# Kernel tuning notes

Hardware: AMD Instinct MI355X
Metric: run time of the kernel (lower is better)

The kernel has to match this reference:

```python
import jax, jax.numpy as jnp
from jax import lax
import numpy as np

B, C, HH, WW = 8, 64, 128, 128
N = HH * WW
EPS = 1e-5


def _roll_h(xn, sign):
    # per-channel cyclic roll along H: out[b,c,h,w] = xn[b,c,(h - sign*c) % H, w]
    _, Cx, Hx, _ = xn.shape
    c = jnp.arange(Cx)[:, None]
    idx = (jnp.arange(Hx)[None, :] - sign * jnp.arange(Cx)[:, None]) % Hx  # (C,H)
    return xn[:, c, idx, :]


def _roll_w(xn, sign):
    return _roll_h(xn.transpose(0, 1, 3, 2), sign).transpose(0, 1, 3, 2)


def _ch_linear(xn, w, b):
    # nn.Linear over the channel dim of a BCHW tensor (token-MLP on (B,N,C))
    return jnp.einsum('bchw,cd->bdhw', xn, w) + b[None, :, None, None]


def _bn(xn, g, b):
    # BatchNorm2d, training-mode stats (biased var over B,H,W)
    m = xn.mean(axis=(0, 2, 3), keepdims=True)
    v = xn.var(axis=(0, 2, 3), keepdims=True)
    return (xn - m) * lax.rsqrt(v + EPS) * g[None, :, None, None] + b[None, :, None, None]


def _dwconv(xn, w, dil, pad):
    return lax.conv_general_dilated(xn, w, (1, 1), ((pad, pad), (pad, pad)),
                                    rhs_dilation=(dil, dil),
                                    dimension_numbers=('NCHW', 'OIHW', 'NCHW'),
                                    feature_group_count=xn.shape[1])


def _pc(xn, w):
    # 1x1 pointwise conv, no bias; w: (C_out, C_in)
    return jnp.einsum('bchw,oc->bohw', xn, w)


def lgff_forward(x, fc1_w, fc1_b, fc2_w, fc2_b, fc3_w, fc3_b, fc4_w, fc4_b,
                 fc5_w, fc5_b, ln_g, ln_b, pc_w, dw_w, dw_b, dw_bn_g, dw_bn_b,
                 dd_w, dd_bn_g, dd_bn_b, se_w1, se_b1, se_w2, se_b2, H, W):
    Bx, Nx, Cx = x.shape
    xn = x.transpose(0, 2, 1).reshape(Bx, Cx, H, W)
    # branch 1: roll+c along H -> fc1 -> GELU -> roll+c along W -> fc2
    a = jax.nn.gelu(_ch_linear(_roll_h(xn, 1), fc1_w, fc1_b), approximate=False)
    x_1 = _ch_linear(_roll_w(a, 1), fc2_w, fc2_b) + xn
    # branch 2: roll-c along W -> fc3 -> GELU -> roll+c along H -> fc4
    b = jax.nn.gelu(_ch_linear(_roll_w(xn, -1), fc3_w, fc3_b), approximate=False)
    x_2 = _ch_linear(_roll_h(b, 1), fc4_w, fc4_b) + xn
    # concat along feature dim (token layout dim=2 == channel dim here), LayerNorm(2C), fc5
    xc = jnp.concatenate([x_1, x_2], axis=1)  # (B, 2C, H, W)
    m = xc.mean(axis=1, keepdims=True)
    v = xc.var(axis=1, keepdims=True)
    xc = (xc - m) * lax.rsqrt(v + EPS) * ln_g[None, :, None, None] + ln_b[None, :, None, None]
    x1 = _ch_linear(xc, fc5_w, fc5_b) + xn
    # conv fusion part
    x2 = _pc(x1, pc_w)
    y = jax.nn.relu(_bn(_dwconv(x2, dw_w, 1, 1) + dw_b[None, :, None, None], dw_bn_g, dw_bn_b))
    y = jax.nn.relu(_bn(_dwconv(y, dd_w, 2, 2), dd_bn_g, dd_bn_b))
    y = _pc(y, pc_w)
    # four branches x3..x6 share identical weights/input -> identical outputs
    x7 = 4.0 * (x2 * y)
    # SE block
    s = x7.mean(axis=(2, 3), keepdims=True)  # (B,C,1,1)
    e = jax.nn.relu(jnp.einsum('bcij,oc->boij', s, se_w1) + se_b1[None, :, None, None])
    e = jax.nn.sigmoid(jnp.einsum('bcij,oc->boij', e, se_w2) + se_b2[None, :, None, None])
    return x7 + x7 * e  # (B, C, H, W)


def setup_inputs():
    key = jax.random.key(0)
    ks = jax.random.split(key, 12)
    r = C // 8
    inp = {
        'x': jax.random.normal(ks[0], (B, N, C), jnp.float32),
        'fc1_w': jax.random.normal(ks[1], (C, C), jnp.float32) * 0.02,
        'fc1_b': jnp.zeros((C,), jnp.float32),
        'fc2_w': jax.random.normal(ks[2], (C, C), jnp.float32) * 0.02,
        'fc2_b': jnp.zeros((C,), jnp.float32),
        'fc3_w': jax.random.normal(ks[3], (C, C), jnp.float32) * 0.02,
        'fc3_b': jnp.zeros((C,), jnp.float32),
        'fc4_w': jax.random.normal(ks[4], (C, C), jnp.float32) * 0.02,
        'fc4_b': jnp.zeros((C,), jnp.float32),
        'fc5_w': jax.random.normal(ks[5], (2 * C, C), jnp.float32) * 0.02,
        'fc5_b': jnp.zeros((C,), jnp.float32),
        'ln_g': jnp.ones((2 * C,), jnp.float32),
        'ln_b': jnp.zeros((2 * C,), jnp.float32),
        'pc_w': jax.random.normal(ks[6], (C, C), jnp.float32) * np.sqrt(2.0 / C).astype(np.float32),
        'dw_w': jax.random.normal(ks[7], (C, 1, 3, 3), jnp.float32) * np.sqrt(2.0 / 9.0).astype(np.float32),
        'dw_b': jnp.zeros((C,), jnp.float32),
        'dw_bn_g': jnp.ones((C,), jnp.float32),
        'dw_bn_b': jnp.zeros((C,), jnp.float32),
        'dd_w': jax.random.normal(ks[8], (C, 1, 3, 3), jnp.float32) * np.sqrt(2.0 / 9.0).astype(np.float32),
        'dd_bn_g': jnp.ones((C,), jnp.float32),
        'dd_bn_b': jnp.zeros((C,), jnp.float32),
        'se_w1': jax.random.normal(ks[9], (r, C), jnp.float32) * np.sqrt(2.0 / r).astype(np.float32),
        'se_b1': jnp.zeros((r,), jnp.float32),
        'se_w2': jax.random.normal(ks[10], (C, r), jnp.float32) * np.sqrt(2.0 / C).astype(np.float32),
        'se_b2': jnp.zeros((C,), jnp.float32),
        'H': HH,
        'W': WW,
    }
    return inp


def reference(x, fc1_w, fc1_b, fc2_w, fc2_b, fc3_w, fc3_b, fc4_w, fc4_b,
              fc5_w, fc5_b, ln_g, ln_b, pc_w, dw_w, dw_b, dw_bn_g, dw_bn_b,
              dd_w, dd_bn_g, dd_bn_b, se_w1, se_b1, se_w2, se_b2, H, W):
    return lgff_forward(x, fc1_w, fc1_b, fc2_w, fc2_b, fc3_w, fc3_b, fc4_w, fc4_b,
                        fc5_w, fc5_b, ln_g, ln_b, pc_w, dw_w, dw_b, dw_bn_g, dw_bn_b,
                        dd_w, dd_bn_g, dd_bn_b, se_w1, se_b1, se_w2, se_b2, H, W)
```

## Files before the change

kernel.cpp:

```cpp
#include <hip/hip_runtime.h>

constexpr int NB  = 8;
constexpr int NC  = 64;
constexpr int NH  = 128;
constexpr int NW  = 128;
constexpr int NHW = NH * NW;
constexpr int CHW = NC * NHW;
constexpr int SZ  = NB * CHW;
constexpr int NPOS = NB * NHW;
constexpr float EPS = 1e-5f;

typedef unsigned short u16;
using bf8   = __attribute__((ext_vector_type(8))) short;
using u16x8 = __attribute__((ext_vector_type(8))) u16;
using f32x4 = __attribute__((ext_vector_type(4))) float;

static __device__ inline short f2bf(float f) {
    union { float f; unsigned int u; } v; v.f = f;
    unsigned int r = v.u + 0x7fffu + ((v.u >> 16) & 1u);
    return (short)(r >> 16);
}
static __device__ inline float bf2f(u16 u) {
    union { unsigned int i; float f; } v; v.i = ((unsigned int)u) << 16;
    return v.f;
}

__global__ void k_transpose(const float* __restrict__ x, u16* __restrict__ xn) {
    __shared__ float t[64 * 65];
    int b   = blockIdx.x >> 8;
    int hw0 = (blockIdx.x & 255) << 6;
    int tid = threadIdx.x;
    #pragma unroll
    for (int k = 0; k < 16; ++k) {
        int idx = tid + (k << 8);
        int c = idx & 63, hwl = idx >> 6;
        t[c * 65 + hwl] = x[((size_t)b * NHW + hw0 + hwl) * NC + c];
    }
    __syncthreads();
    #pragma unroll
    for (int k = 0; k < 16; ++k) {
        int idx = tid + (k << 8);
        int hwl = idx & 63, c = idx >> 6;
        xn[(size_t)(b * NC + c) * NHW + hw0 + hwl] = (u16)f2bf(t[c * 65 + hwl]);
    }
}

template<int MODE, bool GELU_OUT, bool WTRANS, bool HASBIAS, bool BNRELU_IN>
__global__ __launch_bounds__(256) void
k_mfc(const u16* __restrict__ in, const float* __restrict__ wgt,
      const float* __restrict__ bias,
      const float* __restrict__ meanc, const float* __restrict__ rstdc,
      const float* __restrict__ bng, const float* __restrict__ bnb,
      u16* __restrict__ out) {
    __shared__ short wt[64 * 64];
    __shared__ float scl[64], sft[64];
    int tid = threadIdx.x;
    int l = tid & 63, wv = tid >> 6;

    if (!WTRANS) {
        #pragma unroll
        for (int i = 0; i < 8; ++i) {
            int c0 = wv * 2 + i * 8;
            unsigned int pk = (unsigned int)(u16)f2bf(wgt[c0 * 64 + l]) |
                              ((unsigned int)(u16)f2bf(wgt[(c0 + 1) * 64 + l]) << 16);
            *(unsigned int*)&wt[l * 64 + (c0 ^ ((l & 7) << 3))] = pk;
        }
    } else {
        #pragma unroll
        for (int i = 0; i < 16; ++i) {
            int d = wv * 16 + i;
            wt[d * 64 + (l ^ ((d & 7) << 3))] = f2bf(wgt[d * 64 + l]);
        }
    }
    if (BNRELU_IN && tid < 64) {
        float s = rstdc[tid] * bng[tid];
        scl[tid] = s;
        sft[tid] = bnb[tid] - meanc[tid] * s;
    }
    __syncthreads();

    int q = l >> 4, col = l & 15;
    int p  = blockIdx.x * 64 + wv * 16 + col;
    int b  = p >> 14;
    int hw = p & (NHW - 1);
    int h  = hw >> 7, w = hw & 127;
    const u16* inb = in + (size_t)b * CHW;

    f32x4 acc[4];
    #pragma unroll
    for (int dt = 0; dt < 4; ++dt) acc[dt] = (f32x4){0.f, 0.f, 0.f, 0.f};

    #pragma unroll
    for (int ks = 0; ks < 2; ++ks) {
        bf8 bfr;
        #pragma unroll
        for (int j = 0; j < 8; ++j) {
            int c = ks * 32 + q * 8 + j;
            int addr;
            if (MODE == 0)      addr = c * NHW + (((h - c) & 127) << 7) + w;
            else if (MODE == 1) addr = c * NHW + (h << 7) + ((w - c) & 127);
            else if (MODE == 2) addr = c * NHW + (h << 7) + ((w + c) & 127);
            else                addr = c * NHW + hw;
            u16 raw = inb[addr];
            if (BNRELU_IN) {
                float v = fmaxf(bf2f(raw) * scl[c] + sft[c], 0.f);
                bfr[j] = f2bf(v);
            } else {
                bfr[j] = (short)raw;
            }
        }
        #pragma unroll
        for (int dt = 0; dt < 4; ++dt) {
            int d = dt * 16 + col;
            bf8 afr = *(bf8*)&wt[d * 64 + ((ks * 32 + q * 8) ^ ((d & 7) << 3))];
            acc[dt] = __builtin_amdgcn_mfma_f32_16x16x32_bf16(afr, bfr, acc[dt], 0, 0, 0);
        }
    }

    size_t obase = (size_t)b * CHW + hw;
    #pragma unroll
    for (int dt = 0; dt < 4; ++dt) {
        #pragma unroll
        for (int r = 0; r < 4; ++r) {
            int d = dt * 16 + q * 4 + r;
            float val = acc[dt][r];
            if (HASBIAS) val += bias[d];
            if (GELU_OUT) val = 0.5f * val * (1.f + erff(val * 0.70710678118654752f));
            out[obase + (size_t)d * NHW] = (u16)f2bf(val);
        }
    }
}

__global__ void k_pq(const float* __restrict__ w5, const float* __restrict__ lng,
                     const float* __restrict__ lnb, float* __restrict__ PQ) {
    int d = threadIdx.x;
    float P = 0.f, Q = 0.f;
    for (int c = 0; c < 128; ++c) {
        float wv = w5[c * 64 + d];
        P += lng[c] * wv;
        Q += lnb[c] * wv;
    }
    PQ[d] = P; PQ[64 + d] = Q;
}

__global__ __launch_bounds__(256) void
k_ffuse(const u16* __restrict__ t1, const u16* __restrict__ t2,
        const u16* __restrict__ xnb,
        const float* __restrict__ fc2w, const float* __restrict__ fc2b,
        const float* __restrict__ fc4w, const float* __restrict__ fc4b,
        const float* __restrict__ w5, const float* __restrict__ lng,
        const float* __restrict__ PQ, const float* __restrict__ b5,
        u16* __restrict__ x1out) {
    __shared__ short wA[64 * 64];
    __shared__ short wB[64 * 64];
    __shared__ short wG[64 * 128];
    __shared__ short xt[64 * 136];

    int tid = threadIdx.x;
    int l = tid & 63, wv = tid >> 6;

    #pragma unroll
    for (int i = 0; i < 8; ++i) {
        int c0 = wv * 2 + i * 8;
        unsigned int pa = (unsigned int)(u16)f2bf(fc2w[c0 * 64 + l]) |
                          ((unsigned int)(u16)f2bf(fc2w[(c0 + 1) * 64 + l]) << 16);
        *(unsigned int*)&wA[l * 64 + (c0 ^ ((l & 7) << 3))] = pa;
        unsigned int pb = (unsigned int)(u16)f2bf(fc4w[c0 * 64 + l]) |
                          ((unsigned int)(u16)f2bf(fc4w[(c0 + 1) * 64 + l]) << 16);
        *(unsigned int*)&wB[l * 64 + (c0 ^ ((l & 7) << 3))] = pb;
    }
    #pragma unroll
    for (int i = 0; i < 16; ++i) {
        int c0 = wv * 2 + i * 8;
        unsigned int pk = (unsigned int)(u16)f2bf(lng[c0] * w5[c0 * 64 + l]) |
                          ((unsigned int)(u16)f2bf(lng[c0 + 1] * w5[(c0 + 1) * 64 + l]) << 16);
        *(unsigned int*)&wG[l * 128 + (c0 ^ ((l & 7) << 3))] = pk;
    }
    __syncthreads();

    int q = l >> 4, col = l & 15;
    int p  = blockIdx.x * 64 + wv * 16 + col;
    int b  = p >> 14;
    int hw = p & (NHW - 1);
    int h  = hw >> 7, w = hw & 127;
    size_t base = (size_t)b * CHW;
    int pos = wv * 16 + col;

    f32x4 acc1[4], acc2[4];
    #pragma unroll
    for (int dt = 0; dt < 4; ++dt) {
        acc1[dt] = (f32x4){0.f, 0.f, 0.f, 0.f};
        acc2[dt] = (f32x4){0.f, 0.f, 0.f, 0.f};
    }
    #pragma unroll
    for (int ks = 0; ks < 2; ++ks) {
        bf8 f1, f2;
        #pragma unroll
        for (int j = 0; j < 8; ++j) {
            int c = ks * 32 + q * 8 + j;
            f1[j] = (short)t1[base + c * NHW + (h << 7) + ((w - c) & 127)];
            f2[j] = (short)t2[base + c * NHW + (((h - c) & 127) << 7) + w];
        }
        #pragma unroll
        for (int dt = 0; dt < 4; ++dt) {
            int d = dt * 16 + col;
            int wo = (ks * 32 + q * 8) ^ ((d & 7) << 3);
            acc1[dt] = __builtin_amdgcn_mfma_f32_16x16x32_bf16(*(bf8*)&wA[d * 64 + wo], f1, acc1[dt], 0, 0, 0);
            acc2[dt] = __builtin_amdgcn_mfma_f32_16x16x32_bf16(*(bf8*)&wB[d * 64 + wo], f2, acc2[dt], 0, 0, 0);
        }
    }

    float xr[16];
    #pragma unroll
    for (int dt = 0; dt < 4; ++dt)
        #pragma unroll
        for (int r = 0; r < 4; ++r)
            xr[dt * 4 + r] = bf2f(xnb[base + (size_t)(dt * 16 + q * 4 + r) * NHW + hw]);

    float s = 0.f, sq = 0.f;
    #pragma unroll
    for (int dt = 0; dt < 4; ++dt) {
        float v1[4], v2[4];
        #pragma unroll
        for (int r = 0; r < 4; ++r) {
            int d = dt * 16 + q * 4 + r;
            v1[r] = acc1[dt][r] + fc2b[d] + xr[dt * 4 + r];
            v2[r] = acc2[dt][r] + fc4b[d] + xr[dt * 4 + r];
            s += v1[r] + v2[r];
            sq += v1[r] * v1[r] + v2[r] * v2[r];
        }
        unsigned int pk0 = (unsigned int)(u16)f2bf(v1[0]) | ((unsigned int)(u16)f2bf(v1[1]) << 16);
        unsigned int pk1 = (unsigned int)(u16)f2bf(v1[2]) | ((unsigned int)(u16)f2bf(v1[3]) << 16);
        *(uint2*)&xt[pos * 136 + dt * 16 + q * 4] = make_uint2(pk0, pk1);
        unsigned int pk2 = (unsigned int)(u16)f2bf(v2[0]) | ((unsigned int)(u16)f2bf(v2[1]) << 16);
        unsigned int pk3 = (unsigned int)(u16)f2bf(v2[2]) | ((unsigned int)(u16)f2bf(v2[3]) << 16);
        *(uint2*)&xt[pos * 136 + 64 + dt * 16 + q * 4] = make_uint2(pk2, pk3);
    }
    s  += __shfl_xor(s, 16);  s += __shfl_xor(s, 32);
    sq += __shfl_xor(sq, 16); sq += __shfl_xor(sq, 32);
    float m    = s * (1.f / 128.f);
    float var  = sq * (1.f / 128.f) - m * m;
    float rstd = rsqrtf(var + EPS);
    float mr   = m * rstd;
    __syncthreads();

    f32x4 acc[4];
    #pragma unroll
    for (int dt = 0; dt < 4; ++dt) acc[dt] = (f32x4){0.f, 0.f, 0.f, 0.f};
    #pragma unroll
    for (int ks = 0; ks < 4; ++ks) {
        bf8 bfr = *(bf8*)&xt[pos * 136 + ks * 32 + q * 8];
        #pragma unroll
        for (int dt = 0; dt < 4; ++dt) {
            int d = dt * 16 + col;
            bf8 afr = *(bf8*)&wG[d * 128 + ((ks * 32 + q * 8) ^ ((d & 7) << 3))];
            acc[dt] = __builtin_amdgcn_mfma_f32_16x16x32_bf16(afr, bfr, acc[dt], 0, 0, 0);
        }
    }

    size_t obase = base + hw;
    #pragma unroll
    for (int dt = 0; dt < 4; ++dt) {
        #pragma unroll
        for (int r = 0; r < 4; ++r) {
            int d = dt * 16 + q * 4 + r;
            float val = rstd * acc[dt][r] + PQ[64 + d] - mr * PQ[d] + b5[d] + xr[dt * 4 + r];
            x1out[obase + (size_t)d * NHW] = (u16)f2bf(val);
        }
    }
}

template<int DIL, bool HASBIAS, bool BNIN>
__global__ __launch_bounds__(256) void
k_dwlds(const u16* __restrict__ in, const float* __restrict__ wgt,
        const float* __restrict__ bias,
        const float* __restrict__ meanc, const float* __restrict__ rstdc,
        const float* __restrict__ bng, const float* __restrict__ bnb,
        u16* __restrict__ out, float* __restrict__ psum, float* __restrict__ psq) {
    constexpr int STR = 136;
    __shared__ float tile[36 * STR];
    __shared__ float ss[256], sq[256];

    int blk = ((blockIdx.x & 7) << 8) | (blockIdx.x >> 3);
    int q   = blk & 3;
    int bc  = blk >> 2;
    int c   = bc & 63;
    int r0  = q * 32;
    int tid = threadIdx.x;
    const u16* ip = in + (size_t)bc * NHW;

    float scale = 0.f, shift = 0.f;
    if (BNIN) { scale = rstdc[c] * bng[c]; shift = bnb[c] - meanc[c] * scale; }

    #pragma unroll 1
    for (int idx = tid; idx < 36 * 16; idx += 256) {
        int lr = idx >> 4, u = idx & 15;
        int gr = r0 - 2 + lr;
        float v[8] = {0.f, 0.f, 0.f, 0.f, 0.f, 0.f, 0.f, 0.f};
        if (gr >= 0 && gr < NH) {
            u16x8 raw = *(const u16x8*)(ip + gr * NW + u * 8);
            #pragma unroll
            for (int j = 0; j < 8; ++j) {
                float f = bf2f(raw[j]);
                if (BNIN) f = fmaxf(f * scale + shift, 0.f);
                v[j] = f;
            }
        }
        *(float4*)&tile[lr * STR + 4 + u * 8]     = make_float4(v[0], v[1], v[2], v[3]);
        *(float4*)&tile[lr * STR + 4 + u * 8 + 4] = make_float4(v[4], v[5], v[6], v[7]);
        if (u == 0)  *(float4*)&tile[lr * STR]       = make_float4(0.f, 0.f, 0.f, 0.f);
        if (u == 15) *(float4*)&tile[lr * STR + 132] = make_float4(0.f, 0.f, 0.f, 0.f);
    }
    __syncthreads();

    float wc[9];
    #pragma unroll
    for (int k = 0; k < 9; ++k) wc[k] = wgt[c * 9 + k];

    int row  = tid >> 3;
    int col0 = (tid & 7) * 16;
    float o[16];
    float bb = HASBIAS ? bias[c] : 0.f;
    #pragma unroll
    for (int j = 0; j < 16; ++j) o[j] = bb;

    #pragma unroll
    for (int i = 0; i < 3; ++i) {
        const float* rp = &tile[(row + 2 + (i - 1) * DIL) * STR + 4 + col0];
        float4 A  = *(const float4*)(rp - 4);
        float4 B0 = *(const float4*)(rp);
        float4 B1 = *(const float4*)(rp + 4);
        float4 B2 = *(const float4*)(rp + 8);
        float4 B3 = *(const float4*)(rp + 12);
        float4 Cc = *(const float4*)(rp + 16);
        float ww[24] = {A.x,A.y,A.z,A.w, B0.x,B0.y,B0.z,B0.w, B1.x,B1.y,B1.z,B1.w,
                        B2.x,B2.y,B2.z,B2.w, B3.x,B3.y,B3.z,B3.w, Cc.x,Cc.y,Cc.z,Cc.w};
        float w0 = wc[3 * i], w1 = wc[3 * i + 1], w2 = wc[3 * i + 2];
        #pragma unroll
        for (int j = 0; j < 16; ++j)
            o[j] += w0 * ww[4 + j - DIL] + w1 * ww[4 + j] + w2 * ww[4 + j + DIL];
    }

    u16* op = out + (size_t)bc * NHW + (r0 + row) * NW + col0;
    u16x8 o1, o2;
    #pragma unroll
    for (int j = 0; j < 8; ++j) { o1[j] = (u16)f2bf(o[j]); o2[j] = (u16)f2bf(o[8 + j]); }
    *(u16x8*)(op)     = o1;
    *(u16x8*)(op + 8) = o2;

    float s = 0.f, qq = 0.f;
    #pragma unroll
    for (int j = 0; j < 16; ++j) { s += o[j]; qq += o[j] * o[j]; }
    ss[tid] = s; sq[tid] = qq; __syncthreads();
    for (int off = 128; off > 0; off >>= 1) {
        if (tid < off) { ss[tid] += ss[tid + off]; sq[tid] += sq[tid + off]; }
        __syncthreads();
    }
    if (tid == 0) { psum[blk] = ss[0]; psq[blk] = sq[0]; }
}

__global__ void k_bn_finalize(const float* __restrict__ psum, const float* __restrict__ psq,
                              float* __restrict__ meanc, float* __restrict__ rstdc) {
    int c = threadIdx.x;
    float s = 0.f, qv = 0.f;
    for (int b = 0; b < NB; ++b)
        #pragma unroll
        for (int j = 0; j < 4; ++j) {
            int idx = ((b * 64 + c) << 2) + j;
            s += psum[idx]; qv += psq[idx];
        }
    const float inv = 1.f / (float)(NB * NHW);
    float m = s * inv;
    float v = qv * inv - m * m;
    meanc[c] = m;
    rstdc[c] = rsqrtf(v + EPS);
}

__global__ void k_se_reduce(const u16* __restrict__ x2, const u16* __restrict__ y3,
                            float* __restrict__ s4) {
    __shared__ float ss[256];
    int q   = blockIdx.x & 3;
    int bc  = blockIdx.x >> 2;
    int tid = threadIdx.x;
    const u16* a  = x2 + (size_t)bc * NHW + q * (NHW / 4);
    const u16* b_ = y3 + (size_t)bc * NHW + q * (NHW / 4);
    float acc = 0.f;
    #pragma unroll
    for (int i = 0; i < 2; ++i) {
        u16x8 av = *(const u16x8*)(a + (tid + i * 256) * 8);
        u16x8 bv = *(const u16x8*)(b_ + (tid + i * 256) * 8);
        #pragma unroll
        for (int j = 0; j < 8; ++j) acc += bf2f(av[j]) * bf2f(bv[j]);
    }
    ss[tid] = acc; __syncthreads();
    for (int o = 128; o > 0; o >>= 1) {
        if (tid < o) ss[tid] += ss[tid + o];
        __syncthreads();
    }
    if (tid == 0) s4[blockIdx.x] = ss[0];
}

__global__ void k_se_mlp(const float* __restrict__ s4, const float* __restrict__ w1,
                         const float* __restrict__ b1, const float* __restrict__ w2,
                         const float* __restrict__ b2, float* __restrict__ e) {
    __shared__ float sh[64], e1[8];
    int b = blockIdx.x, tid = threadIdx.x;
    float sv = 0.f;
    #pragma unroll
    for (int j = 0; j < 4; ++j) sv += s4[(b * 64 + tid) * 4 + j];
    sh[tid] = sv * (4.f / (float)NHW);
    __syncthreads();
    if (tid < 8) {
        float a = b1[tid];
        for (int c = 0; c < 64; ++c) a += sh[c] * w1[tid * 64 + c];
        e1[tid] = a > 0.f ? a : 0.f;
    }
    __syncthreads();
    float a = b2[tid];
    #pragma unroll
    for (int j = 0; j < 8; ++j) a += e1[j] * w2[tid * 8 + j];
    e[b * 64 + tid] = 1.f / (1.f + expf(-a));
}

__global__ void k_final8(const u16* __restrict__ x2, const u16* __restrict__ y3,
                         const float* __restrict__ e, float* __restrict__ out) {
    int t  = blockIdx.x * 256 + threadIdx.x;
    int bc = t >> 11;
    float f = 4.f * (1.f + e[bc]);
    u16x8 av = *(const u16x8*)(x2 + (size_t)t * 8);
    u16x8 bv = *(const u16x8*)(y3 + (size_t)t * 8);
    float4 o0, o1;
    o0.x = f * bf2f(av[0]) * bf2f(bv[0]); o0.y = f * bf2f(av[1]) * bf2f(bv[1]);
    o0.z = f * bf2f(av[2]) * bf2f(bv[2]); o0.w = f * bf2f(av[3]) * bf2f(bv[3]);
    o1.x = f * bf2f(av[4]) * bf2f(bv[4]); o1.y = f * bf2f(av[5]) * bf2f(bv[5]);
    o1.z = f * bf2f(av[6]) * bf2f(bv[6]); o1.w = f * bf2f(av[7]) * bf2f(bv[7]);
    *(float4*)(out + (size_t)t * 8)     = o0;
    *(float4*)(out + (size_t)t * 8 + 4) = o1;
}

extern "C" void kernel_launch(void* const* d_in, const int* in_sizes, int n_in,
                              void* d_out, int out_size, void* d_ws, size_t ws_size,
                              hipStream_t stream) {
    const float* x     = (const float*)d_in[0];
    const float* fc1w  = (const float*)d_in[1];
    const float* fc1b  = (const float*)d_in[2];
    const float* fc2w  = (const float*)d_in[3];
    const float* fc2b  = (const float*)d_in[4];
    const float* fc3w  = (const float*)d_in[5];
    const float* fc3b  = (const float*)d_in[6];
    const float* fc4w  = (const float*)d_in[7];
    const float* fc4b  = (const float*)d_in[8];
    const float* fc5w  = (const float*)d_in[9];
    const float* fc5b  = (const float*)d_in[10];
    const float* lng   = (const float*)d_in[11];
    const float* lnb   = (const float*)d_in[12];
    const float* pcw   = (const float*)d_in[13];
    const float* dww   = (const float*)d_in[14];
    const float* dwb   = (const float*)d_in[15];
    const float* dwbng = (const float*)d_in[16];
    const float* dwbnb = (const float*)d_in[17];
    const float* ddw   = (const float*)d_in[18];
    const float* ddbng = (const float*)d_in[19];
    const float* ddbnb = (const float*)d_in[20];
    const float* sew1  = (const float*)d_in[21];
    const float* seb1  = (const float*)d_in[22];
    const float* sew2  = (const float*)d_in[23];
    const float* seb2  = (const float*)d_in[24];

    float* out = (float*)d_out;
    u16* wsu = (u16*)d_ws;
    u16* bufA = wsu;
    u16* bufB = wsu + (size_t)SZ;
    u16* bufC = wsu + (size_t)2 * SZ;
    u16* bufD = wsu + (size_t)3 * SZ;
    float* st = (float*)(wsu + (size_t)4 * SZ);
    float* psumA  = st;
    float* psqA   = st + 2048;
    float* meanc1 = st + 4096;
    float* rstdc1 = st + 4160;
    float* meanc2 = st + 4224;
    float* rstdc2 = st + 4288;
    float* svec   = st + 4352;
    float* evec   = st + 6400;
    float* pqv    = st + 6912;

    dim3 blk(256);
    const float* nil = nullptr;

    k_transpose<<<NB * (NHW / 64), blk, 0, stream>>>(x, bufA);
    k_pq<<<1, 64, 0, stream>>>(fc5w, lng, lnb, pqv);
    k_mfc<0, true,  false, true, false><<<NPOS / 64, blk, 0, stream>>>(bufA, fc1w, fc1b, nil, nil, nil, nil, bufB);
    k_mfc<2, true,  false, true, false><<<NPOS / 64, blk, 0, stream>>>(bufA, fc3w, fc3b, nil, nil, nil, nil, bufC);
    k_ffuse<<<NPOS / 64, blk, 0, stream>>>(bufB, bufC, bufA, fc2w, fc2b, fc4w, fc4b,
                                           fc5w, lng, pqv, fc5b, bufD);
    k_mfc<3, false, true, false, false><<<NPOS / 64, blk, 0, stream>>>(bufD, pcw, nil, nil, nil, nil, nil, bufA);
    k_dwlds<1, true, false><<<2048, blk, 0, stream>>>(bufA, dww, dwb, nil, nil, nil, nil, bufB, psumA, psqA);
    k_bn_finalize<<<1, 64, 0, stream>>>(psumA, psqA, meanc1, rstdc1);
    k_dwlds<2, false, true><<<2048, blk, 0, stream>>>(bufB, ddw, nil, meanc1, rstdc1, dwbng, dwbnb, bufC, psumA, psqA);
    k_bn_finalize<<<1, 64, 0, stream>>>(psumA, psqA, meanc2, rstdc2);
    k_mfc<3, false, true, false, true><<<NPOS / 64, blk, 0, stream>>>(bufC, pcw, nil, meanc2, rstdc2, ddbng, ddbnb, bufD);
    k_se_reduce<<<NB * NC * 4, blk, 0, stream>>>(bufA, bufD, svec);
    k_se_mlp<<<NB, 64, 0, stream>>>(svec, sew1, seb1, sew2, seb2, evec);
    k_final8<<<SZ / 2048, blk, 0, stream>>>(bufA, bufD, evec, out);
}
```

Before: 152.8 us.

## Fuse fc1/fc3 into one kernel and fold pointwise conv into ffuse

Merges the two roll+fc+GELU kernels into a single kernel that reads the input once and writes both intermediates. It also appends the 1x1 pointwise conv to the fused fc2/fc4/LayerNorm/fc5 kernel, reusing shared memory for the pc weights so the fc5 output never goes to global memory. Kernel launches and intermediate global traffic both drop. The trade-off is higher register and LDS pressure per block, plus an extra sync, which may lower occupancy.

New measurement: 191.1 us. +25.0%, slower.

```diff
diff --git a/kernel.cpp b/kernel.cpp
--- a/kernel.cpp
+++ b/kernel.cpp
@@ -45,92 +45,6 @@
     }
 }
 
-template<int MODE, bool GELU_OUT, bool WTRANS, bool HASBIAS, bool BNRELU_IN>
-__global__ __launch_bounds__(256) void
-k_mfc(const u16* __restrict__ in, const float* __restrict__ wgt,
-      const float* __restrict__ bias,
-      const float* __restrict__ meanc, const float* __restrict__ rstdc,
-      const float* __restrict__ bng, const float* __restrict__ bnb,
-      u16* __restrict__ out) {
-    __shared__ short wt[64 * 64];
-    __shared__ float scl[64], sft[64];
-    int tid = threadIdx.x;
-    int l = tid & 63, wv = tid >> 6;
-
-    if (!WTRANS) {
-        #pragma unroll
-        for (int i = 0; i < 8; ++i) {
-            int c0 = wv * 2 + i * 8;
-            unsigned int pk = (unsigned int)(u16)f2bf(wgt[c0 * 64 + l]) |
-                              ((unsigned int)(u16)f2bf(wgt[(c0 + 1) * 64 + l]) << 16);
-            *(unsigned int*)&wt[l * 64 + (c0 ^ ((l & 7) << 3))] = pk;
-        }
-    } else {
-        #pragma unroll
-        for (int i = 0; i < 16; ++i) {
-            int d = wv * 16 + i;
-            wt[d * 64 + (l ^ ((d & 7) << 3))] = f2bf(wgt[d * 64 + l]);
-        }
-    }
-    if (BNRELU_IN && tid < 64) {
-        float s = rstdc[tid] * bng[tid];
-        scl[tid] = s;
-        sft[tid] = bnb[tid] - meanc[tid] * s;
-    }
-    __syncthreads();
-
-    int q = l >> 4, col = l & 15;
-    int p  = blockIdx.x * 64 + wv * 16 + col;
-    int b  = p >> 14;
-    int hw = p & (NHW - 1);
-    int h  = hw >> 7, w = hw & 127;
-    const u16* inb = in + (size_t)b * CHW;
-
-    f32x4 acc[4];
-    #pragma unroll
-    for (int dt = 0; dt < 4; ++dt) acc[dt] = (f32x4){0.f, 0.f, 0.f, 0.f};
-
-    #pragma unroll
-    for (int ks = 0; ks < 2; ++ks) {
-        bf8 bfr;
-        #pragma unroll
-        for (int j = 0; j < 8; ++j) {
-            int c = ks * 32 + q * 8 + j;
-            int addr;
-            if (MODE == 0)      addr = c * NHW + (((h - c) & 127) << 7) + w;
-            else if (MODE == 1) addr = c * NHW + (h << 7) + ((w - c) & 127);
-            else if (MODE == 2) addr = c * NHW + (h << 7) + ((w + c) & 127);
-            else                addr = c * NHW + hw;
-            u16 raw = inb[addr];
-            if (BNRELU_IN) {
-                float v = fmaxf(bf2f(raw) * scl[c] + sft[c], 0.f);
-                bfr[j] = f2bf(v);
-            } else {
-                bfr[j] = (short)raw;
-            }
-        }
-        #pragma unroll
-        for (int dt = 0; dt < 4; ++dt) {
-            int d = dt * 16 + col;
-            bf8 afr = *(bf8*)&wt[d * 64 + ((ks * 32 + q * 8) ^ ((d & 7) << 3))];
-            acc[dt] = __builtin_amdgcn_mfma_f32_16x16x32_bf16(afr, bfr, acc[dt], 0, 0, 0);
-        }
-    }
-
-    size_t obase = (size_t)b * CHW + hw;
-    #pragma unroll
-    for (int dt = 0; dt < 4; ++dt) {
-        #pragma unroll
-        for (int r = 0; r < 4; ++r) {
-            int d = dt * 16 + q * 4 + r;
-            float val = acc[dt][r];
-            if (HASBIAS) val += bias[d];
-            if (GELU_OUT) val = 0.5f * val * (1.f + erff(val * 0.70710678118654752f));
-            out[obase + (size_t)d * NHW] = (u16)f2bf(val);
-        }
-    }
-}
-
 __global__ void k_pq(const float* __restrict__ w5, const float* __restrict__ lng,
                      const float* __restrict__ lnb, float* __restrict__ PQ) {
     int d = threadIdx.x;
@@ -144,17 +58,88 @@
 }
 
 __global__ __launch_bounds__(256) void
-k_ffuse(const u16* __restrict__ t1, const u16* __restrict__ t2,
-        const u16* __restrict__ xnb,
-        const float* __restrict__ fc2w, const float* __restrict__ fc2b,
-        const float* __restrict__ fc4w, const float* __restrict__ fc4b,
-        const float* __restrict__ w5, const float* __restrict__ lng,
-        const float* __restrict__ PQ, const float* __restrict__ b5,
-        u16* __restrict__ x1out) {
+k_mfc2(const u16* __restrict__ xn,
+       const float* __restrict__ w1, const float* __restrict__ b1,
+       const float* __restrict__ w3, const float* __restrict__ b3,
+       u16* __restrict__ t1, u16* __restrict__ t2) {
     __shared__ short wA[64 * 64];
     __shared__ short wB[64 * 64];
-    __shared__ short wG[64 * 128];
-    __shared__ short xt[64 * 136];
+    int tid = threadIdx.x;
+    int l = tid & 63, wv = tid >> 6;
+
+    #pragma unroll
+    for (int i = 0; i < 8; ++i) {
+        int c0 = wv * 2 + i * 8;
+        unsigned int pa = (unsigned int)(u16)f2bf(w1[c0 * 64 + l]) |
+                          ((unsigned int)(u16)f2bf(w1[(c0 + 1) * 64 + l]) << 16);
+        *(unsigned int*)&wA[l * 64 + (c0 ^ ((l & 7) << 3))] = pa;
+        unsigned int pb = (unsigned int)(u16)f2bf(w3[c0 * 64 + l]) |
+                          ((unsigned int)(u16)f2bf(w3[(c0 + 1) * 64 + l]) << 16);
+        *(unsigned int*)&wB[l * 64 + (c0 ^ ((l & 7) << 3))] = pb;
+    }
+    __syncthreads();
+
+    int q = l >> 4, col = l & 15;
+    int p  = blockIdx.x * 64 + wv * 16 + col;
+    int b  = p >> 14;
+    int hw = p & (NHW - 1);
+    int h  = hw >> 7, w = hw & 127;
+    const u16* inb = xn + (size_t)b * CHW;
+
+    f32x4 acc1[4], acc2[4];
+    #pragma unroll
+    for (int dt = 0; dt < 4; ++dt) {
+        acc1[dt] = (f32x4){0.f, 0.f, 0.f, 0.f};
+        acc2[dt] = (f32x4){0.f, 0.f, 0.f, 0.f};
+    }
+    #pragma unroll
+    for (int ks = 0; ks < 2; ++ks) {
+        bf8 f1, f2;
+        #pragma unroll
+        for (int j = 0; j < 8; ++j) {
+            int c = ks * 32 + q * 8 + j;
+            f1[j] = (short)inb[c * NHW + (((h - c) & 127) << 7) + w];
+            f2[j] = (short)inb[c * NHW + (h << 7) + ((w + c) & 127)];
+        }
+        #pragma unroll
+        for (int dt = 0; dt < 4; ++dt) {
+            int d = dt * 16 + col;
+            int wo = (ks * 32 + q * 8) ^ ((d & 7) << 3);
+            acc1[dt] = __builtin_amdgcn_mfma_f32_16x16x32_bf16(*(bf8*)&wA[d * 64 + wo], f1, acc1[dt], 0, 0, 0);
+            acc2[dt] = __builtin_amdgcn_mfma_f32_16x16x32_bf16(*(bf8*)&wB[d * 64 + wo], f2, acc2[dt], 0, 0, 0);
+        }
+    }
+
+    size_t obase = (size_t)b * CHW + hw;
+    #pragma unroll
+    for (int dt = 0; dt < 4; ++dt) {
+        #pragma unroll
+        for (int r = 0; r < 4; ++r) {
+            int d = dt * 16 + q * 4 + r;
+            float v1 = acc1[dt][r] + b1[d];
+            v1 = 0.5f * v1 * (1.f + erff(v1 * 0.70710678118654752f));
+            float v2 = acc2[dt][r] + b3[d];
+            v2 = 0.5f * v2 * (1.f + erff(v2 * 0.70710678118654752f));
+            t1[obase + (size_t)d * NHW] = (u16)f2bf(v1);
+            t2[obase + (size_t)d * NHW] = (u16)f2bf(v2);
+        }
+    }
+}
+
+__global__ __launch_bounds__(256) void
+k_ffusepc(const u16* __restrict__ t1, const u16* __restrict__ t2,
+          const u16* __restrict__ xnb,
+          const float* __restrict__ fc2w, const float* __restrict__ fc2b,
+          const float* __restrict__ fc4w, const float* __restrict__ fc4b,
+          const float* __restrict__ w5, const float* __restrict__ lng,
+          const float* __restrict__ PQ, const float* __restrict__ b5,
+          const float* __restrict__ pcw,
+          u16* __restrict__ x2out) {
+    __shared__ short smem[25088];
+    short* wA = smem;
+    short* wB = smem + 4096;
+    short* wG = smem + 8192;
+    short* xt = smem + 16384;
 
     int tid = threadIdx.x;
     int l = tid & 63, wv = tid >> 6;
@@ -242,7 +227,14 @@
     float var  = sq * (1.f / 128.f) - m * m;
     float rstd = rsqrtf(var + EPS);
     float mr   = m * rstd;
-    __syncthreads();
+
+    __syncthreads();
+    short* wP = wA;
+    #pragma unroll
+    for (int i = 0; i < 16; ++i) {
+        int d = wv * 16 + i;
+        wP[d * 64 + (l ^ ((d & 7) << 3))] = f2bf(pcw[d * 64 + l]);
+    }
 
     f32x4 acc[4];
     #pragma unroll
@@ -257,17 +249,108 @@
             acc[dt] = __builtin_amdgcn_mfma_f32_16x16x32_bf16(afr, bfr, acc[dt], 0, 0, 0);
         }
     }
-
-    size_t obase = base + hw;
+    __syncthreads();
+
     #pragma unroll
     for (int dt = 0; dt < 4; ++dt) {
+        float v[4];
         #pragma unroll
         for (int r = 0; r < 4; ++r) {
             int d = dt * 16 + q * 4 + r;
-            float val = rstd * acc[dt][r] + PQ[64 + d] - mr * PQ[d] + b5[d] + xr[dt * 4 + r];
-            x1out[obase + (size_t)d * NHW] = (u16)f2bf(val);
-        }
-    }
+            v[r] = rstd * acc[dt][r] + PQ[64 + d] - mr * PQ[d] + b5[d] + xr[dt * 4 + r];
+        }
+        unsigned int pk0 = (unsigned int)(u16)f2bf(v[0]) | ((unsigned int)(u16)f2bf(v[1]) << 16);
+        unsigned int pk1 = (unsigned int)(u16)f2bf(v[2]) | ((unsigned int)(u16)f2bf(v[3]) << 16);
+        *(uint2*)&xt[pos * 136 + dt * 16 + q * 4] = make_uint2(pk0, pk1);
+    }
+
+    f32x4 accp[4];
+    #pragma unroll
+    for (int dt = 0; dt < 4; ++dt) accp[dt] = (f32x4){0.f, 0.f, 0.f, 0.f};
+    #pragma unroll
+    for (int ks = 0; ks < 2; ++ks) {
+        bf8 bfr = *(bf8*)&xt[pos * 136 + ks * 32 + q * 8];
+        #pragma unroll
+        for (int dt = 0; dt < 4; ++dt) {
+            int d = dt * 16 + col;
+            bf8 afr = *(bf8*)&wP[d * 64 + ((ks * 32 + q * 8) ^ ((d & 7) << 3))];
+            accp[dt] = __builtin_amdgcn_mfma_f32_16x16x32_bf16(afr, bfr, accp[dt], 0, 0, 0);
+        }
+    }
+
+    size_t obase = base + hw;
+    #pragma unroll
+    for (int dt = 0; dt < 4; ++dt)
+        #pragma unroll
+        for (int r = 0; r < 4; ++r) {
+            int d = dt * 16 + q * 4 + r;
+            x2out[obase + (size_t)d * NHW] = (u16)f2bf(accp[dt][r]);
+        }
+}
+
+template<bool BNRELU_IN>
+__global__ __launch_bounds__(256) void
+k_mfc(const u16* __restrict__ in, const float* __restrict__ wgt,
+      const float* __restrict__ meanc, const float* __restrict__ rstdc,
+      const float* __restrict__ bng, const float* __restrict__ bnb,
+      u16* __restrict__ out) {
+    __shared__ short wt[64 * 64];
+    __shared__ float scl[64], sft[64];
+    int tid = threadIdx.x;
+    int l = tid & 63, wv = tid >> 6;
+
+    #pragma unroll
+    for (int i = 0; i < 16; ++i) {
+        int d = wv * 16 + i;
+        wt[d * 64 + (l ^ ((d & 7) << 3))] = f2bf(wgt[d * 64 + l]);
+    }
+    if (BNRELU_IN && tid < 64) {
+        float s = rstdc[tid] * bng[tid];
+        scl[tid] = s;
+        sft[tid] = bnb[tid] - meanc[tid] * s;
+    }
+    __syncthreads();
+
+    int q = l >> 4, col = l & 15;
+    int p  = blockIdx.x * 64 + wv * 16 + col;
+    int b  = p >> 14;
+    int hw = p & (NHW - 1);
+    const u16* inb = in + (size_t)b * CHW;
+
+    f32x4 acc[4];
+    #pragma unroll
+    for (int dt = 0; dt < 4; ++dt) acc[dt] = (f32x4){0.f, 0.f, 0.f, 0.f};
+
+    #pragma unroll
+    for (int ks = 0; ks < 2; ++ks) {
+        bf8 bfr;
+        #pragma unroll
+        for (int j = 0; j < 8; ++j) {
+            int c = ks * 32 + q * 8 + j;
+            u16 raw = inb[c * NHW + hw];
+            if (BNRELU_IN) {
+                float v = fmaxf(bf2f(raw) * scl[c] + sft[c], 0.f);
+                bfr[j] = f2bf(v);
+            } else {
+                bfr[j] = (short)raw;
+            }
+        }
+        #pragma unroll
+        for (int dt = 0; dt < 4; ++dt) {
+            int d = dt * 16 + col;
+            bf8 afr = *(bf8*)&wt[d * 64 + ((ks * 32 + q * 8) ^ ((d & 7) << 3))];
+            acc[dt] = __builtin_amdgcn_mfma_f32_16x16x32_bf16(afr, bfr, acc[dt], 0, 0, 0);
+        }
+    }
+
+    size_t obase = (size_t)b * CHW + hw;
+    #pragma unroll
+    for (int dt = 0; dt < 4; ++dt)
+        #pragma unroll
+        for (int r = 0; r < 4; ++r) {
+            int d = dt * 16 + q * 4 + r;
+            out[obase + (size_t)d * NHW] = (u16)f2bf(acc[dt][r]);
+        }
 }
 
 template<int DIL, bool HASBIAS, bool BNIN>
@@ -489,17 +572,15 @@
 
     k_transpose<<<NB * (NHW / 64), blk, 0, stream>>>(x, bufA);
     k_pq<<<1, 64, 0, stream>>>(fc5w, lng, lnb, pqv);
-    k_mfc<0, true,  false, true, false><<<NPOS / 64, blk, 0, stream>>>(bufA, fc1w, fc1b, nil, nil, nil, nil, bufB);
-    k_mfc<2, true,  false, true, false><<<NPOS / 64, blk, 0, stream>>>(bufA, fc3w, fc3b, nil, nil, nil, nil, bufC);
-    k_ffuse<<<NPOS / 64, blk, 0, stream>>>(bufB, bufC, bufA, fc2w, fc2b, fc4w, fc4b,
-                                           fc5w, lng, pqv, fc5b, bufD);
-    k_mfc<3, false, true, false, false><<<NPOS / 64, blk, 0, stream>>>(bufD, pcw, nil, nil, nil, nil, nil, bufA);
-    k_dwlds<1, true, false><<<2048, blk, 0, stream>>>(bufA, dww, dwb, nil, nil, nil, nil, bufB, psumA, psqA);
+    k_mfc2<<<NPOS / 64, blk, 0, stream>>>(bufA, fc1w, fc1b, fc3w, fc3b, bufB, bufC);
+    k_ffusepc<<<NPOS / 64, blk, 0, stream>>>(bufB, bufC, bufA, fc2w, fc2b, fc4w, fc4b,
+                                             fc5w, lng, pqv, fc5b, pcw, bufD);
+    k_dwlds<1, true, false><<<2048, blk, 0, stream>>>(bufD, dww, dwb, nil, nil, nil, nil, bufB, psumA, psqA);
     k_bn_finalize<<<1, 64, 0, stream>>>(psumA, psqA, meanc1, rstdc1);
     k_dwlds<2, false, true><<<2048, blk, 0, stream>>>(bufB, ddw, nil, meanc1, rstdc1, dwbng, dwbnb, bufC, psumA, psqA);
     k_bn_finalize<<<1, 64, 0, stream>>>(psumA, psqA, meanc2, rstdc2);
-    k_mfc<3, false, true, false, true><<<NPOS / 64, blk, 0, stream>>>(bufC, pcw, nil, meanc2, rstdc2, ddbng, ddbnb, bufD);
-    k_se_reduce<<<NB * NC * 4, blk, 0, stream>>>(bufA, bufD, svec);
+    k_mfc<true><<<NPOS / 64, blk, 0, stream>>>(bufC, pcw, meanc2, rstdc2, ddbng, ddbnb, bufA);
+    k_se_reduce<<<NB * NC * 4, blk, 0, stream>>>(bufD, bufA, svec);
     k_se_mlp<<<NB, 64, 0, stream>>>(svec, sew1, seb1, sew2, seb2, evec);
-    k_final8<<<SZ / 2048, blk, 0, stream>>>(bufA, bufD, evec, out);
-}
+    k_final8<<<SZ / 2048, blk, 0, stream>>>(bufD, bufA, evec, out);
+}
```
